# Kernel tuning notes

Hardware: AMD Instinct MI355X
Metric: run time of the kernel (lower is better)

Reference implementation:

```python
import jax, jax.numpy as jnp
import numpy as np

IN_F = 2048
OUT_F = 2048
BLOCK = 32
N_TOK = 2048
IBLK = IN_F // BLOCK    # 64 block-columns of the weight
OBLK = OUT_F // BLOCK   # 64 block-rows of the weight
NNZ = 1228


def _layout():
    # Deterministic block-sparsity pattern: NNZ distinct (out_block, in_block) pairs.
    rs = np.random.RandomState(0)
    pos = np.sort(rs.permutation(OBLK * IBLK)[:NNZ])
    oi = (pos // IBLK).astype(np.int32)  # output block-row of each nnz block
    ii = (pos % IBLK).astype(np.int32)   # input block-col of each nnz block
    return jnp.asarray(oi), jnp.asarray(ii)


def setup_inputs() -> dict:
    key = jax.random.key(0)
    k1, k2 = jax.random.split(key)
    x = jax.random.normal(k1, (N_TOK, IN_F), dtype=jnp.float32)
    # block values: w[k] is the dense block W[oi[k]*B:(oi[k]+1)*B, ii[k]*B:(ii[k]+1)*B]
    w = jax.random.normal(k2, (NNZ, BLOCK, BLOCK), dtype=jnp.float32) * (1.0 / np.sqrt(IN_F))
    oi, ii = _layout()
    return {"x": x, "w": w, "oi": oi, "ii": ii}


def reference(x, w, oi, ii):
    # Block-sparse linear: y = x @ W^T where W is block-sparse (out, in).
    # DDS matmul: dense x times sparse W, honoring the block layout (no dense W).
    xb = x.reshape(N_TOK, IBLK, BLOCK)          # [N, IBLK, B]
    xg = xb[:, ii, :]                           # gather input blocks -> [N, NNZ, B]
    # per-nnz-block GEMM: y_block[o] += x_block[i] @ W_block[o,i]^T
    contrib = jnp.einsum('nki,koi->kno', xg, w)  # [NNZ, N, B]
    yb = jax.ops.segment_sum(contrib, oi, num_segments=OBLK)  # [OBLK, N, B]
    return jnp.transpose(yb, (1, 0, 2)).reshape(N_TOK, OUT_F)
```

## Files before the change

### kernel.cpp

```cpp
#include <hip/hip_runtime.h>

#define N_TOK 2048
#define IN_FEAT 2048
#define NNZB 1228
#define XN8 ((N_TOK * IN_FEAT) / 8)
#define WN8 ((NNZB * 1024) / 8)

typedef __attribute__((ext_vector_type(8))) short short8;
typedef __attribute__((ext_vector_type(4))) float floatx4;

__device__ __forceinline__ short f2bf(float f) {
  unsigned u = __builtin_bit_cast(unsigned, f);
  u += 0x7FFFu + ((u >> 16) & 1u);
  return (short)(u >> 16);
}

__device__ __forceinline__ short8 cvt8(const float4 a, const float4 b) {
  short8 r;
  r[0] = f2bf(a.x); r[1] = f2bf(a.y); r[2] = f2bf(a.z); r[3] = f2bf(a.w);
  r[4] = f2bf(b.x); r[5] = f2bf(b.y); r[6] = f2bf(b.z); r[7] = f2bf(b.w);
  return r;
}

__global__ __launch_bounds__(256) void cvt_kernel(
    const float* __restrict__ x, const float* __restrict__ w,
    const int* __restrict__ oi,
    short8* __restrict__ xb, short8* __restrict__ wb, int* __restrict__ offs) {
  const int tid = blockIdx.x * 256 + threadIdx.x;
  if (blockIdx.x == 0 && threadIdx.x < 65) {
    const int target = threadIdx.x;
    int lo = 0, hi = NNZB;
    while (lo < hi) { int m = (lo + hi) >> 1; if (oi[m] < target) lo = m + 1; else hi = m; }
    offs[threadIdx.x] = lo;
  }
  if (tid < XN8) {
    const float4* p = (const float4*)x + (size_t)tid * 2;
    xb[tid] = cvt8(p[0], p[1]);
  } else if (tid < XN8 + WN8) {
    const int t = tid - XN8;
    const float4* p = (const float4*)w + (size_t)t * 2;
    wb[t] = cvt8(p[0], p[1]);
  }
}

template <int USE_WS>
__global__ __launch_bounds__(256, 4) void bsl_main(
    const short8* __restrict__ xb, const short8* __restrict__ wb,
    const int* __restrict__ offs,
    const float* __restrict__ x, const float* __restrict__ w,
    const int* __restrict__ oi, const int* __restrict__ ii,
    float* __restrict__ y) {
  const int ob   = blockIdx.x >> 5;
  const int tile = blockIdx.x & 31;
  const int lane = threadIdx.x & 63;
  const int wv   = __builtin_amdgcn_readfirstlane(threadIdx.x >> 6);
  const int row16 = lane & 15;
  const int kgrp  = lane >> 4;

  __shared__ float red[2][64 * 32];

  int e0, e1;
  if (USE_WS) {
    e0 = offs[ob];
    e1 = offs[ob + 1];
  } else {
    int lo = 0, hi = NNZB;
    while (lo < hi) { int m = (lo + hi) >> 1; if (oi[m] < ob) lo = m + 1; else hi = m; }
    e0 = lo;
    hi = NNZB;
    while (lo < hi) { int m = (lo + hi) >> 1; if (oi[m] < ob + 1) lo = m + 1; else hi = m; }
    e1 = lo;
  }
  const int cnt = e1 - e0;
  const int ks = e0 + (cnt * wv) / 4;
  const int ke = e0 + (cnt * (wv + 1)) / 4;

  const int tokBase = tile * 64;

  floatx4 acc[4][2] = {};

  if (USE_WS) {
    const short8* xrow = xb + (size_t)(tokBase + row16) * 256 + kgrp;
    #pragma unroll 2
    for (int k = ks; k < ke; ++k) {
      const int ib = ii[k];
      short8 b0 = wb[(size_t)k * 128 + row16 * 4 + kgrp];
      short8 b1 = wb[(size_t)k * 128 + (row16 + 16) * 4 + kgrp];
      const short8* xp = xrow + ib * 4;
      #pragma unroll
      for (int m = 0; m < 4; ++m) {
        short8 a = xp[m * 16 * 256];
        acc[m][0] = __builtin_amdgcn_mfma_f32_16x16x32_bf16(a, b0, acc[m][0], 0, 0, 0);
        acc[m][1] = __builtin_amdgcn_mfma_f32_16x16x32_bf16(a, b1, acc[m][1], 0, 0, 0);
      }
    }
  } else {
    const float* xrow = x + (size_t)(tokBase + row16) * IN_FEAT + kgrp * 8;
    #pragma unroll 2
    for (int k = ks; k < ke; ++k) {
      const int ib = ii[k];
      const float* wbp = w + (size_t)k * 1024 + kgrp * 8;
      const float4* wp0 = (const float4*)(wbp + row16 * 32);
      const float4* wp1 = (const float4*)(wbp + (row16 + 16) * 32);
      short8 b0 = cvt8(wp0[0], wp0[1]);
      short8 b1 = cvt8(wp1[0], wp1[1]);
      const float* xp = xrow + ib * 32;
      #pragma unroll
      for (int m = 0; m < 4; ++m) {
        const float4* ap = (const float4*)(xp + (size_t)(m * 16) * IN_FEAT);
        short8 a = cvt8(ap[0], ap[1]);
        acc[m][0] = __builtin_amdgcn_mfma_f32_16x16x32_bf16(a, b0, acc[m][0], 0, 0, 0);
        acc[m][1] = __builtin_amdgcn_mfma_f32_16x16x32_bf16(a, b1, acc[m][1], 0, 0, 0);
      }
    }
  }

  {
    float* b0p = red[0];
    float* b1p = red[1];
    if (wv == 1 || wv == 3) {
      float* b = (wv == 1) ? b0p : b1p;
      #pragma unroll
      for (int m = 0; m < 4; ++m)
        #pragma unroll
        for (int nf = 0; nf < 2; ++nf)
          #pragma unroll
          for (int r = 0; r < 4; ++r)
            b[(m * 16 + kgrp * 4 + r) * 32 + nf * 16 + row16] = acc[m][nf][r];
    }
    __syncthreads();
    if (wv == 0 || wv == 2) {
      const float* b = (wv == 0) ? b0p : b1p;
      #pragma unroll
      for (int m = 0; m < 4; ++m)
        #pragma unroll
        for (int nf = 0; nf < 2; ++nf)
          #pragma unroll
          for (int r = 0; r < 4; ++r)
            acc[m][nf][r] += b[(m * 16 + kgrp * 4 + r) * 32 + nf * 16 + row16];
    }
    __syncthreads();
    if (wv == 2) {
      #pragma unroll
      for (int m = 0; m < 4; ++m)
        #pragma unroll
        for (int nf = 0; nf < 2; ++nf)
          #pragma unroll
          for (int r = 0; r < 4; ++r)
            b0p[(m * 16 + kgrp * 4 + r) * 32 + nf * 16 + row16] = acc[m][nf][r];
    }
    __syncthreads();
    if (wv == 0) {
      #pragma unroll
      for (int m = 0; m < 4; ++m)
        #pragma unroll
        for (int nf = 0; nf < 2; ++nf)
          #pragma unroll
          for (int r = 0; r < 4; ++r) {
            float v = acc[m][nf][r] + b0p[(m * 16 + kgrp * 4 + r) * 32 + nf * 16 + row16];
            const int row = tokBase + m * 16 + kgrp * 4 + r;
            const int col = ob * 32 + nf * 16 + row16;
            y[(size_t)row * 2048 + col] = v;
          }
    }
  }
}

extern "C" void kernel_launch(void* const* d_in, const int* in_sizes, int n_in,
                              void* d_out, int out_size, void* d_ws, size_t ws_size,
                              hipStream_t stream) {
  const float* x  = (const float*)d_in[0];
  const float* w  = (const float*)d_in[1];
  const int*   oi = (const int*)d_in[2];
  const int*   ii = (const int*)d_in[3];
  float* y = (float*)d_out;

  const size_t need = (size_t)(XN8 + WN8) * 16 + 65 * sizeof(int);
  if (ws_size >= need) {
    short8* xb = (short8*)d_ws;
    short8* wb = xb + XN8;
    int* offs = (int*)(wb + WN8);
    cvt_kernel<<<dim3((XN8 + WN8 + 255) / 256), dim3(256), 0, stream>>>(x, w, oi, xb, wb, offs);
    bsl_main<1><<<dim3(2048), dim3(256), 0, stream>>>(xb, wb, offs, x, w, oi, ii, y);
  } else {
    bsl_main<0><<<dim3(2048), dim3(256), 0, stream>>>(nullptr, nullptr, nullptr, x, w, oi, ii, y);
  }
}
```

Baseline: 105.6 us.

## Double-buffer block loads in registers and rotate per-wave nnz iteration order

The main MFMA loop now prefetches the next nnz block's weight and x fragments into a second register set while the current block's MFMAs run. Block column indices are loaded once per wave and read back with readlane, so each iteration no longer issues its own global load for them. Each tile's waves take a rotated quarter of the block row and start at a staggered offset, so concurrent workgroups touch different x and w blocks and contend less for the same cache lines. The cost is higher register pressure from two buffer sets, and the non-workspace fallback path now also reads the workspace pointers, which are null in that path.

```diff
diff --git a/kernel.cpp b/kernel.cpp
--- a/kernel.cpp
+++ b/kernel.cpp
@@ -72,47 +72,75 @@
     e1 = lo;
   }
   const int cnt = e1 - e0;
-  const int ks = e0 + (cnt * wv) / 4;
-  const int ke = e0 + (cnt * (wv + 1)) / 4;
+
+  const int safek = (lane < cnt) ? (e0 + lane) : 0;
+  const int iiv = ii[safek];
+
+  const int q   = (wv + tile) & 3;
+  const int js  = (cnt * q) >> 2;
+  const int je  = (cnt * (q + 1)) >> 2;
+  const int len = je - js;
+  const int rot = (len > 0) ? ((((tile >> 2) & 7) * len) >> 3) : 0;
 
   const int tokBase = tile * 64;
 
   floatx4 acc[4][2] = {};
 
-  if (USE_WS) {
+  if (len > 0) {
     const short8* xrow = xb + (size_t)(tokBase + row16) * 256 + kgrp;
-    #pragma unroll 2
-    for (int k = ks; k < ke; ++k) {
-      const int ib = ii[k];
-      short8 b0 = wb[(size_t)k * 128 + row16 * 4 + kgrp];
-      short8 b1 = wb[(size_t)k * 128 + (row16 + 16) * 4 + kgrp];
-      const short8* xp = xrow + ib * 4;
-      #pragma unroll
-      for (int m = 0; m < 4; ++m) {
-        short8 a = xp[m * 16 * 256];
-        acc[m][0] = __builtin_amdgcn_mfma_f32_16x16x32_bf16(a, b0, acc[m][0], 0, 0, 0);
-        acc[m][1] = __builtin_amdgcn_mfma_f32_16x16x32_bf16(a, b1, acc[m][1], 0, 0, 0);
-      }
-    }
-  } else {
-    const float* xrow = x + (size_t)(tokBase + row16) * IN_FEAT + kgrp * 8;
-    #pragma unroll 2
-    for (int k = ks; k < ke; ++k) {
-      const int ib = ii[k];
-      const float* wbp = w + (size_t)k * 1024 + kgrp * 8;
-      const float4* wp0 = (const float4*)(wbp + row16 * 32);
-      const float4* wp1 = (const float4*)(wbp + (row16 + 16) * 32);
-      short8 b0 = cvt8(wp0[0], wp0[1]);
-      short8 b1 = cvt8(wp1[0], wp1[1]);
-      const float* xp = xrow + ib * 32;
-      #pragma unroll
-      for (int m = 0; m < 4; ++m) {
-        const float4* ap = (const float4*)(xp + (size_t)(m * 16) * IN_FEAT);
-        short8 a = cvt8(ap[0], ap[1]);
-        acc[m][0] = __builtin_amdgcn_mfma_f32_16x16x32_bf16(a, b0, acc[m][0], 0, 0, 0);
-        acc[m][1] = __builtin_amdgcn_mfma_f32_16x16x32_bf16(a, b1, acc[m][1], 0, 0, 0);
-      }
-    }
+
+    short8 b0A, b1A, a0A, a1A, a2A, a3A;
+    short8 b0B, b1B, a0B, a1B, a2B, a3B;
+
+#define JJ(r_) ({ int rr_ = (r_) + rot; if (rr_ >= len) rr_ -= len; js + rr_; })
+
+#define LD(j_, b0_, b1_, a0_, a1_, a2_, a3_)                                   \
+  {                                                                            \
+    const int j__ = (j_);                                                      \
+    const int k__ = e0 + j__;                                                  \
+    const int ib__ = (j__ < 64) ? __builtin_amdgcn_readlane(iiv, j__)          \
+                                : ii[k__];                                     \
+    const short8* wp__ = wb + (size_t)k__ * 128 + row16 * 4 + kgrp;            \
+    b0_ = wp__[0];                                                             \
+    b1_ = wp__[64];                                                            \
+    const short8* xp__ = xrow + ib__ * 4;                                      \
+    a0_ = xp__[0];                                                             \
+    a1_ = xp__[16 * 256];                                                      \
+    a2_ = xp__[32 * 256];                                                      \
+    a3_ = xp__[48 * 256];                                                      \
+  }
+
+#define FMA(b0_, b1_, a0_, a1_, a2_, a3_)                                      \
+  {                                                                            \
+    acc[0][0] = __builtin_amdgcn_mfma_f32_16x16x32_bf16(a0_, b0_, acc[0][0], 0, 0, 0); \
+    acc[0][1] = __builtin_amdgcn_mfma_f32_16x16x32_bf16(a0_, b1_, acc[0][1], 0, 0, 0); \
+    acc[1][0] = __builtin_amdgcn_mfma_f32_16x16x32_bf16(a1_, b0_, acc[1][0], 0, 0, 0); \
+    acc[1][1] = __builtin_amdgcn_mfma_f32_16x16x32_bf16(a1_, b1_, acc[1][1], 0, 0, 0); \
+    acc[2][0] = __builtin_amdgcn_mfma_f32_16x16x32_bf16(a2_, b0_, acc[2][0], 0, 0, 0); \
+    acc[2][1] = __builtin_amdgcn_mfma_f32_16x16x32_bf16(a2_, b1_, acc[2][1], 0, 0, 0); \
+    acc[3][0] = __builtin_amdgcn_mfma_f32_16x16x32_bf16(a3_, b0_, acc[3][0], 0, 0, 0); \
+    acc[3][1] = __builtin_amdgcn_mfma_f32_16x16x32_bf16(a3_, b1_, acc[3][1], 0, 0, 0); \
+  }
+
+    LD(JJ(0), b0A, b1A, a0A, a1A, a2A, a3A);
+    int r = 0;
+    while (r + 2 <= len - 1) {
+      LD(JJ(r + 1), b0B, b1B, a0B, a1B, a2B, a3B);
+      FMA(b0A, b1A, a0A, a1A, a2A, a3A);
+      LD(JJ(r + 2), b0A, b1A, a0A, a1A, a2A, a3A);
+      FMA(b0B, b1B, a0B, a1B, a2B, a3B);
+      r += 2;
+    }
+    if (r < len - 1) {
+      LD(JJ(r + 1), b0B, b1B, a0B, a1B, a2B, a3B);
+      FMA(b0A, b1A, a0A, a1A, a2A, a3A);
+      FMA(b0B, b1B, a0B, a1B, a2B, a3B);
+    } else {
+      FMA(b0A, b1A, a0A, a1A, a2A, a3A);
+    }
+#undef JJ
+#undef LD
+#undef FMA
   }
 
   {
```

Result: no change. 105.8 us (+0.2%).

## Store bf16 x block-column-major and preload block indices into lanes

Applied to the files above, without the earlier changes.

The conversion kernel now writes the bf16 copy of x grouped by input block (block-major, then token), so each 32-wide input block is a contiguous slab of rows. In the main loop the A loads for a 64-token tile then cover a contiguous 4 KB region instead of rows strided by 4 KB. The per-iteration scalar load of ii[k] is replaced by one vector load of up to 64 indices, read back with readlane. The cost is a scattered read pattern in the conversion kernel, plus a fallback path for rows with more than 64 nonzero blocks.

```diff
diff --git a/kernel.cpp b/kernel.cpp
--- a/kernel.cpp
+++ b/kernel.cpp
@@ -34,7 +34,10 @@
     offs[threadIdx.x] = lo;
   }
   if (tid < XN8) {
-    const float4* p = (const float4*)x + (size_t)tid * 2;
+    const int cg  = tid & 3;
+    const int tok = (tid >> 2) & (N_TOK - 1);
+    const int ib  = tid >> 13;
+    const float4* p = (const float4*)x + ((size_t)tok * 512 + ib * 8 + cg * 2);
     xb[tid] = cvt8(p[0], p[1]);
   } else if (tid < XN8 + WN8) {
     const int t = tid - XN8;
@@ -72,24 +75,30 @@
     e1 = lo;
   }
   const int cnt = e1 - e0;
-  const int ks = e0 + (cnt * wv) / 4;
-  const int ke = e0 + (cnt * (wv + 1)) / 4;
+
+  const int safek = (lane < cnt) ? (e0 + lane) : 0;
+  const int iiv = ii[safek];
+
+  const int ks = (cnt * wv) >> 2;
+  const int ke = (cnt * (wv + 1)) >> 2;
 
   const int tokBase = tile * 64;
 
   floatx4 acc[4][2] = {};
 
   if (USE_WS) {
-    const short8* xrow = xb + (size_t)(tokBase + row16) * 256 + kgrp;
+    const short8* xbase = xb + (size_t)(tokBase + row16) * 4 + kgrp;
     #pragma unroll 2
-    for (int k = ks; k < ke; ++k) {
-      const int ib = ii[k];
-      short8 b0 = wb[(size_t)k * 128 + row16 * 4 + kgrp];
-      short8 b1 = wb[(size_t)k * 128 + (row16 + 16) * 4 + kgrp];
-      const short8* xp = xrow + ib * 4;
+    for (int j = ks; j < ke; ++j) {
+      const int k = e0 + j;
+      const int ib = (j < 64) ? __builtin_amdgcn_readlane(iiv, j) : ii[k];
+      const short8* wp = wb + (size_t)k * 128 + row16 * 4 + kgrp;
+      short8 b0 = wp[0];
+      short8 b1 = wp[64];
+      const short8* xp = xbase + (size_t)ib * 8192;
       #pragma unroll
       for (int m = 0; m < 4; ++m) {
-        short8 a = xp[m * 16 * 256];
+        short8 a = xp[m * 64];
         acc[m][0] = __builtin_amdgcn_mfma_f32_16x16x32_bf16(a, b0, acc[m][0], 0, 0, 0);
         acc[m][1] = __builtin_amdgcn_mfma_f32_16x16x32_bf16(a, b1, acc[m][1], 0, 0, 0);
       }
@@ -97,8 +106,9 @@
   } else {
     const float* xrow = x + (size_t)(tokBase + row16) * IN_FEAT + kgrp * 8;
     #pragma unroll 2
-    for (int k = ks; k < ke; ++k) {
-      const int ib = ii[k];
+    for (int j = ks; j < ke; ++j) {
+      const int k = e0 + j;
+      const int ib = (j < 64) ? __builtin_amdgcn_readlane(iiv, j) : ii[k];
       const float* wbp = w + (size_t)k * 1024 + kgrp * 8;
       const float4* wp0 = (const float4*)(wbp + row16 * 32);
       const float4* wp1 = (const float4*)(wbp + (row16 + 16) * 32);
```

After: 96.28 us. 8.8% less time.
